# Kernel optimization log

Measured on AMD Instinct MI355X. Metric: run time of the kernel, lower is better.

Reference implementation:

```python
import jax, jax.numpy as jnp
import numpy as np

N = 10000          # nodes
E = 160000         # edges (before self-loops)
F_IN = 256
H, C = 8, 64       # heads, channels per head
NUM_CLASSES = 40
NEG_SLOPE = 0.2    # PyG GATConv default leaky_relu slope


def setup_inputs() -> dict:
    key = jax.random.key(0)
    ks = jax.random.split(key, 16)
    s = 0.1  # keep logits tame
    x = jax.random.normal(ks[0], (N, F_IN), jnp.float32)
    edge_index = jax.random.randint(ks[1], (2, E), 0, N)
    W0 = jax.random.normal(ks[2], (F_IN, H * C), jnp.float32) / np.sqrt(F_IN)
    a_src0 = jax.random.normal(ks[3], (H, C), jnp.float32) * s
    a_dst0 = jax.random.normal(ks[4], (H, C), jnp.float32) * s
    b0 = jnp.zeros((H * C,), jnp.float32)
    W1 = jax.random.normal(ks[5], (H * C, H * C), jnp.float32) / np.sqrt(H * C)
    a_src1 = jax.random.normal(ks[6], (H, C), jnp.float32) * s
    a_dst1 = jax.random.normal(ks[7], (H, C), jnp.float32) * s
    b1 = jnp.zeros((H * C,), jnp.float32)
    W2 = jax.random.normal(ks[8], (H * C, NUM_CLASSES), jnp.float32) / np.sqrt(H * C)
    a_src2 = jax.random.normal(ks[9], (1, NUM_CLASSES), jnp.float32) * s
    a_dst2 = jax.random.normal(ks[10], (1, NUM_CLASSES), jnp.float32) * s
    b2 = jnp.zeros((NUM_CLASSES,), jnp.float32)
    return dict(x=x, edge_index=edge_index, W0=W0, a_src0=a_src0, a_dst0=a_dst0, b0=b0,
                W1=W1, a_src1=a_src1, a_dst1=a_dst1, b1=b1,
                W2=W2, a_src2=a_src2, a_dst2=a_dst2, b2=b2)


def gat_conv(x, src, dst, W, a_src, a_dst, b, concat):
    """PyG GATConv (eval mode: dropout = identity)."""
    n = x.shape[0]
    h, c = a_src.shape
    hx = (x @ W).reshape(n, h, c)                       # [N,H,C]
    al_s = jnp.sum(hx * a_src, axis=-1)                 # [N,H]
    al_d = jnp.sum(hx * a_dst, axis=-1)                 # [N,H]
    e = jax.nn.leaky_relu(al_s[src] + al_d[dst], NEG_SLOPE)  # [E,H]
    # neighbor softmax over incoming edges of each dst node
    m = jax.ops.segment_max(e, dst, num_segments=n)     # [N,H]
    ex = jnp.exp(e - m[dst])
    denom = jax.ops.segment_sum(ex, dst, num_segments=n)
    alpha = ex / (denom[dst] + 1e-16)                   # [E,H]
    msg = hx[src] * alpha[:, :, None]                   # [E,H,C]
    out = jax.ops.segment_sum(msg, dst, num_segments=n) # [N,H,C]
    out = out.reshape(n, h * c) if concat else out.mean(axis=1)
    return out + b


def reference(x, edge_index, W0, a_src0, a_dst0, b0, W1, a_src1, a_dst1, b1,
              W2, a_src2, a_dst2, b2):
    # add self-loops once (PyG GATConv add_self_loops=True)
    loops = jnp.arange(N, dtype=edge_index.dtype)
    src = jnp.concatenate([edge_index[0], loops])
    dst = jnp.concatenate([edge_index[1], loops])
    x = jax.nn.elu(gat_conv(x, src, dst, W0, a_src0, a_dst0, b0, True))
    x = jax.nn.elu(gat_conv(x, src, dst, W1, a_src1, a_dst1, b1, True))
    return gat_conv(x, src, dst, W2, a_src2, a_dst2, b2, False)
```

## Files before the change

### kernel.cpp

```cpp
#include <hip/hip_runtime.h>
#include <math.h>

#define NN 10000
#define EE 160000
#define ET 170000
#define FIN 256
#define HH 8
#define HC 512
#define NCLS 40
#define ELLW 96

typedef _Float16 f16;
using f16x8 = __attribute__((ext_vector_type(8))) _Float16;
using f32x4 = __attribute__((ext_vector_type(4))) float;

#define MFMA16(a, b, c) __builtin_amdgcn_mfma_f32_16x16x32_f16((a), (b), (c), 0, 0, 0)

__device__ __forceinline__ void fmamix2(float& alo, float& ahi, unsigned pk, float w) {
    asm("v_fma_mix_f32 %0, %1, %2, %0 op_sel:[0,0,0] op_sel_hi:[1,0,0]"
        : "+v"(alo) : "v"(pk), "v"(w));
    asm("v_fma_mix_f32 %0, %1, %2, %0 op_sel:[1,0,0] op_sel_hi:[1,0,0]"
        : "+v"(ahi) : "v"(pk), "v"(w));
}

__global__ __launch_bounds__(256) void prep0(const float* __restrict__ W0,
                                             f16* __restrict__ w0T,
                                             int* __restrict__ cnt) {
    int i = blockIdx.x * 256 + threadIdx.x;
    if (i < NN) cnt[i] = 0;
    if (i < HC * FIN) {
        int n = i >> 8, k = i & 255;
        w0T[i] = (f16)W0[(size_t)k * HC + n];
    }
}

__global__ __launch_bounds__(512) void mega0(const float* __restrict__ x,
                                             const f16* __restrict__ w0T,
                                             const float* __restrict__ a_src,
                                             const float* __restrict__ a_dst,
                                             const int* __restrict__ ei,
                                             const float* __restrict__ W1,
                                             const float* __restrict__ W2,
                                             f16* __restrict__ hx2,
                                             float* __restrict__ al_s,
                                             float* __restrict__ al_d,
                                             int* __restrict__ cnt,
                                             int* __restrict__ ell,
                                             f16* __restrict__ w1T,
                                             f16* __restrict__ w2T) {
    __shared__ f16 Bs[64 * FIN];
    int b = blockIdx.x;
    int t = threadIdx.x;
    if (b >= 316) {
        if (b < 649) {
            int e = (b - 316) * 512 + t;
            if (e < ET) {
                int s, d;
                if (e < EE) { s = ei[e]; d = ei[EE + e]; }
                else        { s = e - EE; d = s; }
                int pos = atomicAdd(&cnt[d], 1);
                if (pos < ELLW) ell[(size_t)d * ELLW + pos] = s;
            }
        } else if (b < 1161) {
            int j = (b - 649) * 512 + t;
            int n = j >> 9, k = j & 511;
            w1T[j] = (f16)W1[(size_t)k * HC + n];
        } else {
            int j = (b - 1161) * 512 + t;
            if (j < NCLS * HC) {
                int n = j >> 9, k = j & 511;
                w2T[j] = (f16)W2[(size_t)k * NCLS + n];
            }
        }
        return;
    }
    int hp = b & 3, chunk = b >> 2;
    int lane = t & 63, w = t >> 6;
    int fm = lane & 15, g = lane >> 4;
    int bm = chunk * 128 + w * 16;
    int row = bm + fm;
    bool rok = row < NN;

    f16x8 af[8];
#pragma unroll
    for (int kk = 0; kk < 8; ++kk) {
        float4 lo = make_float4(0.f, 0.f, 0.f, 0.f), hi = lo;
        if (rok) {
            const float* ap = x + (size_t)row * FIN + kk * 32 + g * 8;
            lo = *(const float4*)ap;
            hi = *(const float4*)(ap + 4);
        }
        f16x8 v;
        v[0] = (f16)lo.x; v[1] = (f16)lo.y; v[2] = (f16)lo.z; v[3] = (f16)lo.w;
        v[4] = (f16)hi.x; v[5] = (f16)hi.y; v[6] = (f16)hi.z; v[7] = (f16)hi.w;
        af[kk] = v;
    }

    for (int sl = 0; sl < 2; ++sl) {
        int h = hp * 2 + sl;
        const f16* bsrc = w0T + (size_t)h * 64 * FIN;
        for (int c = t; c < 64 * 32; c += 512) {
            int brow = c >> 5, j = c & 31;
            uint4 v = *(const uint4*)(bsrc + (size_t)brow * FIN + j * 8);
            *(uint4*)&Bs[(size_t)brow * FIN + ((j ^ (brow & 7)) * 8)] = v;
        }
        __syncthreads();

        f32x4 acc[4] = {};
#pragma unroll
        for (int kk = 0; kk < 8; ++kk) {
#pragma unroll
            for (int nt = 0; nt < 4; ++nt) {
                f16x8 bb = *(const f16x8*)
                    &Bs[(nt * 16 + fm) * FIN + (((kk * 4 + g) ^ (fm & 7)) * 8)];
                acc[nt] = MFMA16(af[kk], bb, acc[nt]);
            }
        }

        float asc[4], adc[4];
#pragma unroll
        for (int nt = 0; nt < 4; ++nt) {
            asc[nt] = a_src[h * 64 + nt * 16 + fm];
            adc[nt] = a_dst[h * 64 + nt * 16 + fm];
        }
#pragma unroll
        for (int r = 0; r < 4; ++r) {
            int orow = bm + g * 4 + r;
            float s = acc[0][r] * asc[0] + acc[1][r] * asc[1] +
                      acc[2][r] * asc[2] + acc[3][r] * asc[3];
            float d = acc[0][r] * adc[0] + acc[1][r] * adc[1] +
                      acc[2][r] * adc[2] + acc[3][r] * adc[3];
#pragma unroll
            for (int off = 1; off < 16; off <<= 1) {
                s += __shfl_xor(s, off);
                d += __shfl_xor(d, off);
            }
            if (orow < NN) {
                if (fm == 0) {
                    al_s[orow * 8 + h] = s;
                    al_d[orow * 8 + h] = d;
                }
#pragma unroll
                for (int nt = 0; nt < 4; ++nt)
                    hx2[(size_t)orow * HC + h * 64 + nt * 16 + fm] =
                        (f16)acc[nt][r];
            }
        }
        __syncthreads();
    }
}

template <int K>
__global__ __launch_bounds__(512) void gemm_attn(const f16* __restrict__ A,
                                                 const f16* __restrict__ BT,
                                                 const float* __restrict__ a_src,
                                                 const float* __restrict__ a_dst,
                                                 f16* __restrict__ hx2,
                                                 float* __restrict__ al_s,
                                                 float* __restrict__ al_d) {
    constexpr int KK = K / 32;
    constexpr int CH = K / 8;
    __shared__ f16 Bs[64 * K];
    int t = threadIdx.x;
    int hp = blockIdx.x;
    int lane = t & 63, w = t >> 6;
    int fm = lane & 15, g = lane >> 4;
    int bm = blockIdx.y * 128 + w * 16;
    int row = bm + fm;
    bool rok = row < NN;

    f16x8 af[KK];
#pragma unroll
    for (int kk = 0; kk < KK; ++kk) {
        uint4 r = rok ? *(const uint4*)(A + (size_t)row * K + kk * 32 + g * 8)
                      : make_uint4(0u, 0u, 0u, 0u);
        af[kk] = __builtin_bit_cast(f16x8, r);
    }

    for (int sl = 0; sl < 2; ++sl) {
        int h = hp * 2 + sl;
        const f16* bsrc = BT + (size_t)h * 64 * K;
        for (int c = t; c < 64 * CH; c += 512) {
            int brow = c / CH;
            int j = c - brow * CH;
            uint4 v = *(const uint4*)(bsrc + (size_t)brow * K + j * 8);
            *(uint4*)&Bs[(size_t)brow * K + ((j ^ (brow & 7)) * 8)] = v;
        }
        __syncthreads();

        f32x4 acc[4] = {};
#pragma unroll
        for (int kk = 0; kk < KK; ++kk) {
#pragma unroll
            for (int nt = 0; nt < 4; ++nt) {
                f16x8 b = *(const f16x8*)
                    &Bs[(nt * 16 + fm) * K + (((kk * 4 + g) ^ (fm & 7)) * 8)];
                acc[nt] = MFMA16(af[kk], b, acc[nt]);
            }
        }

        float asc[4], adc[4];
#pragma unroll
        for (int nt = 0; nt < 4; ++nt) {
            asc[nt] = a_src[h * 64 + nt * 16 + fm];
            adc[nt] = a_dst[h * 64 + nt * 16 + fm];
        }
#pragma unroll
        for (int r = 0; r < 4; ++r) {
            int orow = bm + g * 4 + r;
            float s = acc[0][r] * asc[0] + acc[1][r] * asc[1] +
                      acc[2][r] * asc[2] + acc[3][r] * asc[3];
            float d = acc[0][r] * adc[0] + acc[1][r] * adc[1] +
                      acc[2][r] * adc[2] + acc[3][r] * adc[3];
#pragma unroll
            for (int off = 1; off < 16; off <<= 1) {
                s += __shfl_xor(s, off);
                d += __shfl_xor(d, off);
            }
            if (orow < NN) {
                if (fm == 0) {
                    al_s[orow * 8 + h] = s;
                    al_d[orow * 8 + h] = d;
                }
#pragma unroll
                for (int nt = 0; nt < 4; ++nt)
                    hx2[(size_t)orow * HC + h * 64 + nt * 16 + fm] =
                        (f16)acc[nt][r];
            }
        }
        __syncthreads();
    }
}

__global__ __launch_bounds__(256) void gemm2_attn(const f16* __restrict__ A,
                                                  const f16* __restrict__ BT,
                                                  const float* __restrict__ a_src2,
                                                  const float* __restrict__ a_dst2,
                                                  float* __restrict__ hx40,
                                                  float* __restrict__ als2,
                                                  float* __restrict__ ald2) {
    __shared__ f16 Bs[48 * HC];
    int t = threadIdx.x;
    int lane = t & 63, w = t >> 6;
    int fm = lane & 15, g = lane >> 4;
    int bm = blockIdx.x * 64 + w * 16;
    int row = bm + fm;
    bool rok = row < NN;

    for (int c = t; c < 48 * 64; c += 256) {
        int brow = c >> 6, j = c & 63;
        uint4 v = make_uint4(0u, 0u, 0u, 0u);
        if (brow < NCLS) v = *(const uint4*)(BT + (size_t)brow * HC + j * 8);
        *(uint4*)&Bs[brow * HC + ((j ^ (brow & 7)) * 8)] = v;
    }

    f16x8 af[16];
#pragma unroll
    for (int kk = 0; kk < 16; ++kk) {
        uint4 r = rok ? *(const uint4*)(A + (size_t)row * HC + kk * 32 + g * 8)
                      : make_uint4(0u, 0u, 0u, 0u);
        af[kk] = __builtin_bit_cast(f16x8, r);
    }
    __syncthreads();

    f32x4 acc[3] = {};
#pragma unroll
    for (int kk = 0; kk < 16; ++kk) {
#pragma unroll
        for (int nt = 0; nt < 3; ++nt) {
            f16x8 b = *(const f16x8*)
                &Bs[(nt * 16 + fm) * HC + (((kk * 4 + g) ^ (fm & 7)) * 8)];
            acc[nt] = MFMA16(af[kk], b, acc[nt]);
        }
    }

    float a2s[3], a2d[3];
#pragma unroll
    for (int nt = 0; nt < 3; ++nt) {
        int col = nt * 16 + fm;
        a2s[nt] = (col < NCLS) ? a_src2[col] : 0.f;
        a2d[nt] = (col < NCLS) ? a_dst2[col] : 0.f;
    }
#pragma unroll
    for (int r = 0; r < 4; ++r) {
        int orow = bm + g * 4 + r;
        float s = acc[0][r] * a2s[0] + acc[1][r] * a2s[1] + acc[2][r] * a2s[2];
        float d = acc[0][r] * a2d[0] + acc[1][r] * a2d[1] + acc[2][r] * a2d[2];
#pragma unroll
        for (int off = 1; off < 16; off <<= 1) {
            s += __shfl_xor(s, off);
            d += __shfl_xor(d, off);
        }
        if (orow < NN) {
            if (fm == 0) { als2[orow] = s; ald2[orow] = d; }
#pragma unroll
            for (int nt = 0; nt < 3; ++nt) {
                int col = nt * 16 + fm;
                if (col < NCLS) hx40[(size_t)orow * NCLS + col] = acc[nt][r];
            }
        }
    }
}

__global__ __launch_bounds__(256) void agg_ell(const f16* __restrict__ hx2,
                                               const float* __restrict__ al_s,
                                               const float* __restrict__ al_d,
                                               const int* __restrict__ cnt,
                                               const int* __restrict__ ell,
                                               const float* __restrict__ bias,
                                               f16* __restrict__ outF) {
    __shared__ float accbuf[2][64][8];
    __shared__ float denbuf[2][64];
    int t = threadIdx.x;
    int lane = t & 63, w = t >> 6;
    int p = w >> 1, sub = w & 1;
    int n = blockIdx.x * 2 + p;
    bool nok = n < NN;
    int ch = lane * 8;
    int h = lane >> 3;
    float acc[8] = {0.f, 0.f, 0.f, 0.f, 0.f, 0.f, 0.f, 0.f};
    float den = 0.f;
    if (nok) {
        float ald = al_d[n * HH + h];
        int dg = cnt[n]; if (dg > ELLW) dg = ELLW;
        const int* ep = ell + (size_t)n * ELLW;
        int nq = dg >> 2;
        for (int q = sub; q < nq; q += 2) {
            int4 ss = *(const int4*)(ep + (q << 2));
            float e0 = al_s[ss.x * HH + h], e1 = al_s[ss.y * HH + h];
            float e2 = al_s[ss.z * HH + h], e3 = al_s[ss.w * HH + h];
            uint4 v0 = *(const uint4*)(hx2 + (size_t)ss.x * HC + ch);
            uint4 v1 = *(const uint4*)(hx2 + (size_t)ss.y * HC + ch);
            uint4 v2 = *(const uint4*)(hx2 + (size_t)ss.z * HC + ch);
            uint4 v3 = *(const uint4*)(hx2 + (size_t)ss.w * HC + ch);
            e0 += ald; e0 = e0 > 0.f ? e0 : 0.2f * e0;
            e1 += ald; e1 = e1 > 0.f ? e1 : 0.2f * e1;
            e2 += ald; e2 = e2 > 0.f ? e2 : 0.2f * e2;
            e3 += ald; e3 = e3 > 0.f ? e3 : 0.2f * e3;
            float w0 = __expf(e0), w1 = __expf(e1);
            float w2 = __expf(e2), w3 = __expf(e3);
            unsigned q0[4] = {v0.x, v0.y, v0.z, v0.w};
            unsigned q1[4] = {v1.x, v1.y, v1.z, v1.w};
            unsigned q2[4] = {v2.x, v2.y, v2.z, v2.w};
            unsigned q3[4] = {v3.x, v3.y, v3.z, v3.w};
#pragma unroll
            for (int j = 0; j < 4; ++j) {
                fmamix2(acc[2 * j], acc[2 * j + 1], q0[j], w0);
                fmamix2(acc[2 * j], acc[2 * j + 1], q1[j], w1);
                fmamix2(acc[2 * j], acc[2 * j + 1], q2[j], w2);
                fmamix2(acc[2 * j], acc[2 * j + 1], q3[j], w3);
            }
            den += w0 + w1 + w2 + w3;
        }
        if (sub == (nq & 1)) {
            for (int i2 = nq << 2; i2 < dg; ++i2) {
                int s = ep[i2];
                float e = al_s[s * HH + h] + ald;
                e = e > 0.f ? e : 0.2f * e;
                float wgt = __expf(e);
                uint4 v = *(const uint4*)(hx2 + (size_t)s * HC + ch);
                unsigned qq[4] = {v.x, v.y, v.z, v.w};
#pragma unroll
                for (int j = 0; j < 4; ++j)
                    fmamix2(acc[2 * j], acc[2 * j + 1], qq[j], wgt);
                den += wgt;
            }
        }
    }
    if (sub == 1) {
#pragma unroll
        for (int j = 0; j < 8; ++j) accbuf[p][lane][j] = acc[j];
        denbuf[p][lane] = den;
    }
    __syncthreads();
    if (sub == 0 && nok) {
#pragma unroll
        for (int j = 0; j < 8; ++j) acc[j] += accbuf[p][lane][j];
        den += denbuf[p][lane];
        float inv = 1.f / (den + 1e-16f);
        float4 b0v = *(const float4*)(bias + ch);
        float4 b1v = *(const float4*)(bias + ch + 4);
        float bb[8] = {b0v.x, b0v.y, b0v.z, b0v.w, b1v.x, b1v.y, b1v.z, b1v.w};
        f16x8 o;
#pragma unroll
        for (int j = 0; j < 8; ++j) {
            float v = acc[j] * inv + bb[j];
            v = v > 0.f ? v : expm1f(v);
            o[j] = (f16)v;
        }
        *(uint4*)(outF + (size_t)n * HC + ch) = __builtin_bit_cast(uint4, o);
    }
}

__global__ __launch_bounds__(256) void agg2_final(const float* __restrict__ hx40,
                                                  const float* __restrict__ als,
                                                  const float* __restrict__ aldp,
                                                  const int* __restrict__ cnt,
                                                  const int* __restrict__ ell,
                                                  const float* __restrict__ b2,
                                                  float* __restrict__ out) {
    int t = threadIdx.x;
    int n = blockIdx.x * 4 + (t >> 6);
    int c = t & 63;
    if (n >= NN) return;
    float ald = aldp[n];
    int dg = cnt[n]; if (dg > ELLW) dg = ELLW;
    const int* ep = ell + (size_t)n * ELLW;
    float acc = 0.f, den = 0.f;
    int i = 0;
    for (; i + 4 <= dg; i += 4) {
        int4 ss = *(const int4*)(ep + i);
        float e0 = als[ss.x], e1 = als[ss.y], e2 = als[ss.z], e3 = als[ss.w];
        float v0 = 0.f, v1 = 0.f, v2 = 0.f, v3 = 0.f;
        if (c < NCLS) {
            v0 = hx40[(size_t)ss.x * NCLS + c];
            v1 = hx40[(size_t)ss.y * NCLS + c];
            v2 = hx40[(size_t)ss.z * NCLS + c];
            v3 = hx40[(size_t)ss.w * NCLS + c];
        }
        e0 += ald; e0 = e0 > 0.f ? e0 : 0.2f * e0;
        e1 += ald; e1 = e1 > 0.f ? e1 : 0.2f * e1;
        e2 += ald; e2 = e2 > 0.f ? e2 : 0.2f * e2;
        e3 += ald; e3 = e3 > 0.f ? e3 : 0.2f * e3;
        float w0 = __expf(e0), w1 = __expf(e1), w2 = __expf(e2), w3 = __expf(e3);
        acc += w0 * v0 + w1 * v1 + w2 * v2 + w3 * v3;
        den += w0 + w1 + w2 + w3;
    }
    for (; i < dg; ++i) {
        int s = ep[i];
        float e = als[s] + ald;
        e = e > 0.f ? e : 0.2f * e;
        float wgt = __expf(e);
        if (c < NCLS) acc += wgt * hx40[(size_t)s * NCLS + c];
        den += wgt;
    }
    if (c < NCLS) out[(size_t)n * NCLS + c] = acc / (den + 1e-16f) + b2[c];
}

extern "C" void kernel_launch(void* const* d_in, const int* in_sizes, int n_in,
                              void* d_out, int out_size, void* d_ws, size_t ws_size,
                              hipStream_t stream) {
    const float* x   = (const float*)d_in[0];
    const int*   ei  = (const int*)  d_in[1];
    const float* W0  = (const float*)d_in[2];
    const float* as0 = (const float*)d_in[3];
    const float* ad0 = (const float*)d_in[4];
    const float* b0  = (const float*)d_in[5];
    const float* W1  = (const float*)d_in[6];
    const float* as1 = (const float*)d_in[7];
    const float* ad1 = (const float*)d_in[8];
    const float* b1  = (const float*)d_in[9];
    const float* W2  = (const float*)d_in[10];
    const float* as2 = (const float*)d_in[11];
    const float* ad2 = (const float*)d_in[12];
    const float* b2  = (const float*)d_in[13];
    float* out = (float*)d_out;

    char* p = (char*)d_ws;
    int* cnt  = (int*)p; p += 40064;
    int* ell  = (int*)p; p += (size_t)NN * ELLW * 4;
    f16* w0T  = (f16*)p; p += HC * FIN * 2;
    f16* w1T  = (f16*)p; p += HC * HC * 2;
    f16* w2T  = (f16*)p; p += NCLS * HC * 2;
    f16* hxA  = (f16*)p; p += (size_t)NN * HC * 2;
    f16* hxB  = (f16*)p; p += (size_t)NN * HC * 2;
    f16* fA   = (f16*)p; p += (size_t)NN * HC * 2;
    f16* fB   = (f16*)p; p += (size_t)NN * HC * 2;
    float* hx40 = (float*)p; p += (size_t)NN * NCLS * 4;
    float* als0 = (float*)p; p += NN * HH * 4;
    float* ald0 = (float*)p; p += NN * HH * 4;
    float* als1 = (float*)p; p += NN * HH * 4;
    float* ald1 = (float*)p; p += NN * HH * 4;
    float* als2 = (float*)p; p += NN * 4;
    float* ald2 = (float*)p; p += NN * 4;

    const int NBR = (NN + 127) / 128;
    const int NAG = (NN + 1) / 2;
    const int NB2 = (NN + 63) / 64;

    prep0<<<(HC * FIN + 255) / 256, 256, 0, stream>>>(W0, w0T, cnt);
    mega0<<<1201, 512, 0, stream>>>(x, w0T, as0, ad0, ei, W1, W2,
                                    hxA, als0, ald0, cnt, ell, w1T, w2T);
    agg_ell<<<NAG, 256, 0, stream>>>(hxA, als0, ald0, cnt, ell, b0, fA);
    dim3 gA(4, NBR);
    gemm_attn<HC><<<gA, 512, 0, stream>>>(fA, w1T, as1, ad1, hxB, als1, ald1);
    agg_ell<<<NAG, 256, 0, stream>>>(hxB, als1, ald1, cnt, ell, b1, fB);
    gemm2_attn<<<NB2, 256, 0, stream>>>(fB, w2T, as2, ad2, hx40, als2, ald2);
    agg2_final<<<(NN + 3) / 4, 256, 0, stream>>>(hx40, als2, ald2, cnt, ell, b2, out);
}
```

Baseline: 199.3 us.

## Fuse aggregation with following GEMM via per-chunk completion counters

Merges each ELL aggregation kernel with the following dense GEMM+attention kernel into one launch. Aggregation blocks (4 nodes each, 512 threads) bump a per-128-row chunk counter, and GEMM blocks spin on that counter before consuming the rows, so the GEMM can start on finished chunks while aggregation continues. This removes two kernel launches and the drain gaps between them. The cost is spin-wait polling, a reliance on aggregation blocks being scheduled before the waiting GEMM blocks, and the GEMM staging its weights in two K-halves to fit the shared-memory union.

After: 465.4 us. +133.5%, slower.

```diff
diff --git a/kernel.cpp b/kernel.cpp
--- a/kernel.cpp
+++ b/kernel.cpp
@@ -9,6 +9,8 @@
 #define HC 512
 #define NCLS 40
 #define ELLW 96
+#define NAGB 2500
+#define NCH 79
 
 typedef _Float16 f16;
 using f16x8 = __attribute__((ext_vector_type(8))) _Float16;
@@ -25,9 +27,12 @@
 
 __global__ __launch_bounds__(256) void prep0(const float* __restrict__ W0,
                                              f16* __restrict__ w0T,
-                                             int* __restrict__ cnt) {
+                                             int* __restrict__ cnt,
+                                             int* __restrict__ cd1,
+                                             int* __restrict__ cd2) {
     int i = blockIdx.x * 256 + threadIdx.x;
     if (i < NN) cnt[i] = 0;
+    if (i < NCH) { cd1[i] = 0; cd2[i] = 0; }
     if (i < HC * FIN) {
         int n = i >> 8, k = i & 255;
         w0T[i] = (f16)W0[(size_t)k * HC + n];
@@ -150,233 +155,84 @@
     }
 }
 
-template <int K>
-__global__ __launch_bounds__(512) void gemm_attn(const f16* __restrict__ A,
-                                                 const f16* __restrict__ BT,
-                                                 const float* __restrict__ a_src,
-                                                 const float* __restrict__ a_dst,
-                                                 f16* __restrict__ hx2,
-                                                 float* __restrict__ al_s,
-                                                 float* __restrict__ al_d) {
-    constexpr int KK = K / 32;
-    constexpr int CH = K / 8;
-    __shared__ f16 Bs[64 * K];
-    int t = threadIdx.x;
-    int hp = blockIdx.x;
-    int lane = t & 63, w = t >> 6;
-    int fm = lane & 15, g = lane >> 4;
-    int bm = blockIdx.y * 128 + w * 16;
-    int row = bm + fm;
-    bool rok = row < NN;
-
-    f16x8 af[KK];
-#pragma unroll
-    for (int kk = 0; kk < KK; ++kk) {
-        uint4 r = rok ? *(const uint4*)(A + (size_t)row * K + kk * 32 + g * 8)
-                      : make_uint4(0u, 0u, 0u, 0u);
-        af[kk] = __builtin_bit_cast(f16x8, r);
-    }
-
-    for (int sl = 0; sl < 2; ++sl) {
-        int h = hp * 2 + sl;
-        const f16* bsrc = BT + (size_t)h * 64 * K;
-        for (int c = t; c < 64 * CH; c += 512) {
-            int brow = c / CH;
-            int j = c - brow * CH;
-            uint4 v = *(const uint4*)(bsrc + (size_t)brow * K + j * 8);
-            *(uint4*)&Bs[(size_t)brow * K + ((j ^ (brow & 7)) * 8)] = v;
-        }
-        __syncthreads();
-
-        f32x4 acc[4] = {};
-#pragma unroll
-        for (int kk = 0; kk < KK; ++kk) {
-#pragma unroll
-            for (int nt = 0; nt < 4; ++nt) {
-                f16x8 b = *(const f16x8*)
-                    &Bs[(nt * 16 + fm) * K + (((kk * 4 + g) ^ (fm & 7)) * 8)];
-                acc[nt] = MFMA16(af[kk], b, acc[nt]);
-            }
-        }
-
-        float asc[4], adc[4];
-#pragma unroll
-        for (int nt = 0; nt < 4; ++nt) {
-            asc[nt] = a_src[h * 64 + nt * 16 + fm];
-            adc[nt] = a_dst[h * 64 + nt * 16 + fm];
-        }
-#pragma unroll
-        for (int r = 0; r < 4; ++r) {
-            int orow = bm + g * 4 + r;
-            float s = acc[0][r] * asc[0] + acc[1][r] * asc[1] +
-                      acc[2][r] * asc[2] + acc[3][r] * asc[3];
-            float d = acc[0][r] * adc[0] + acc[1][r] * adc[1] +
-                      acc[2][r] * adc[2] + acc[3][r] * adc[3];
-#pragma unroll
-            for (int off = 1; off < 16; off <<= 1) {
-                s += __shfl_xor(s, off);
-                d += __shfl_xor(d, off);
-            }
-            if (orow < NN) {
-                if (fm == 0) {
-                    al_s[orow * 8 + h] = s;
-                    al_d[orow * 8 + h] = d;
-                }
-#pragma unroll
-                for (int nt = 0; nt < 4; ++nt)
-                    hx2[(size_t)orow * HC + h * 64 + nt * 16 + fm] =
-                        (f16)acc[nt][r];
-            }
-        }
-        __syncthreads();
-    }
-}
-
-__global__ __launch_bounds__(256) void gemm2_attn(const f16* __restrict__ A,
-                                                  const f16* __restrict__ BT,
-                                                  const float* __restrict__ a_src2,
-                                                  const float* __restrict__ a_dst2,
-                                                  float* __restrict__ hx40,
-                                                  float* __restrict__ als2,
-                                                  float* __restrict__ ald2) {
-    __shared__ f16 Bs[48 * HC];
-    int t = threadIdx.x;
-    int lane = t & 63, w = t >> 6;
-    int fm = lane & 15, g = lane >> 4;
-    int bm = blockIdx.x * 64 + w * 16;
-    int row = bm + fm;
-    bool rok = row < NN;
-
-    for (int c = t; c < 48 * 64; c += 256) {
-        int brow = c >> 6, j = c & 63;
-        uint4 v = make_uint4(0u, 0u, 0u, 0u);
-        if (brow < NCLS) v = *(const uint4*)(BT + (size_t)brow * HC + j * 8);
-        *(uint4*)&Bs[brow * HC + ((j ^ (brow & 7)) * 8)] = v;
-    }
-
-    f16x8 af[16];
-#pragma unroll
-    for (int kk = 0; kk < 16; ++kk) {
-        uint4 r = rok ? *(const uint4*)(A + (size_t)row * HC + kk * 32 + g * 8)
-                      : make_uint4(0u, 0u, 0u, 0u);
-        af[kk] = __builtin_bit_cast(f16x8, r);
-    }
-    __syncthreads();
-
-    f32x4 acc[3] = {};
-#pragma unroll
-    for (int kk = 0; kk < 16; ++kk) {
-#pragma unroll
-        for (int nt = 0; nt < 3; ++nt) {
-            f16x8 b = *(const f16x8*)
-                &Bs[(nt * 16 + fm) * HC + (((kk * 4 + g) ^ (fm & 7)) * 8)];
-            acc[nt] = MFMA16(af[kk], b, acc[nt]);
-        }
-    }
-
-    float a2s[3], a2d[3];
-#pragma unroll
-    for (int nt = 0; nt < 3; ++nt) {
-        int col = nt * 16 + fm;
-        a2s[nt] = (col < NCLS) ? a_src2[col] : 0.f;
-        a2d[nt] = (col < NCLS) ? a_dst2[col] : 0.f;
-    }
-#pragma unroll
-    for (int r = 0; r < 4; ++r) {
-        int orow = bm + g * 4 + r;
-        float s = acc[0][r] * a2s[0] + acc[1][r] * a2s[1] + acc[2][r] * a2s[2];
-        float d = acc[0][r] * a2d[0] + acc[1][r] * a2d[1] + acc[2][r] * a2d[2];
-#pragma unroll
-        for (int off = 1; off < 16; off <<= 1) {
-            s += __shfl_xor(s, off);
-            d += __shfl_xor(d, off);
-        }
-        if (orow < NN) {
-            if (fm == 0) { als2[orow] = s; ald2[orow] = d; }
-#pragma unroll
-            for (int nt = 0; nt < 3; ++nt) {
-                int col = nt * 16 + fm;
-                if (col < NCLS) hx40[(size_t)orow * NCLS + col] = acc[nt][r];
-            }
-        }
-    }
-}
-
-__global__ __launch_bounds__(256) void agg_ell(const f16* __restrict__ hx2,
-                                               const float* __restrict__ al_s,
-                                               const float* __restrict__ al_d,
-                                               const int* __restrict__ cnt,
-                                               const int* __restrict__ ell,
-                                               const float* __restrict__ bias,
-                                               f16* __restrict__ outF) {
-    __shared__ float accbuf[2][64][8];
-    __shared__ float denbuf[2][64];
+struct SM {
+    union {
+        f16 Bs[64 * 256];
+        struct { float ab[4][64][8]; float db[4][64]; } a;
+    } u;
+};
+
+__device__ __forceinline__ void agg_body(SM& sm,
+                                         const f16* __restrict__ hx2,
+                                         const float* __restrict__ al_s,
+                                         const float* __restrict__ al_d,
+                                         const int* __restrict__ cnt,
+                                         const int* __restrict__ ell,
+                                         const float* __restrict__ bias,
+                                         f16* __restrict__ outF, int b) {
     int t = threadIdx.x;
     int lane = t & 63, w = t >> 6;
     int p = w >> 1, sub = w & 1;
-    int n = blockIdx.x * 2 + p;
-    bool nok = n < NN;
+    int n = b * 4 + p;
     int ch = lane * 8;
     int h = lane >> 3;
     float acc[8] = {0.f, 0.f, 0.f, 0.f, 0.f, 0.f, 0.f, 0.f};
     float den = 0.f;
-    if (nok) {
-        float ald = al_d[n * HH + h];
-        int dg = cnt[n]; if (dg > ELLW) dg = ELLW;
-        const int* ep = ell + (size_t)n * ELLW;
-        int nq = dg >> 2;
-        for (int q = sub; q < nq; q += 2) {
-            int4 ss = *(const int4*)(ep + (q << 2));
-            float e0 = al_s[ss.x * HH + h], e1 = al_s[ss.y * HH + h];
-            float e2 = al_s[ss.z * HH + h], e3 = al_s[ss.w * HH + h];
-            uint4 v0 = *(const uint4*)(hx2 + (size_t)ss.x * HC + ch);
-            uint4 v1 = *(const uint4*)(hx2 + (size_t)ss.y * HC + ch);
-            uint4 v2 = *(const uint4*)(hx2 + (size_t)ss.z * HC + ch);
-            uint4 v3 = *(const uint4*)(hx2 + (size_t)ss.w * HC + ch);
-            e0 += ald; e0 = e0 > 0.f ? e0 : 0.2f * e0;
-            e1 += ald; e1 = e1 > 0.f ? e1 : 0.2f * e1;
-            e2 += ald; e2 = e2 > 0.f ? e2 : 0.2f * e2;
-            e3 += ald; e3 = e3 > 0.f ? e3 : 0.2f * e3;
-            float w0 = __expf(e0), w1 = __expf(e1);
-            float w2 = __expf(e2), w3 = __expf(e3);
-            unsigned q0[4] = {v0.x, v0.y, v0.z, v0.w};
-            unsigned q1[4] = {v1.x, v1.y, v1.z, v1.w};
-            unsigned q2[4] = {v2.x, v2.y, v2.z, v2.w};
-            unsigned q3[4] = {v3.x, v3.y, v3.z, v3.w};
-#pragma unroll
-            for (int j = 0; j < 4; ++j) {
-                fmamix2(acc[2 * j], acc[2 * j + 1], q0[j], w0);
-                fmamix2(acc[2 * j], acc[2 * j + 1], q1[j], w1);
-                fmamix2(acc[2 * j], acc[2 * j + 1], q2[j], w2);
-                fmamix2(acc[2 * j], acc[2 * j + 1], q3[j], w3);
-            }
-            den += w0 + w1 + w2 + w3;
-        }
-        if (sub == (nq & 1)) {
-            for (int i2 = nq << 2; i2 < dg; ++i2) {
-                int s = ep[i2];
-                float e = al_s[s * HH + h] + ald;
-                e = e > 0.f ? e : 0.2f * e;
-                float wgt = __expf(e);
-                uint4 v = *(const uint4*)(hx2 + (size_t)s * HC + ch);
-                unsigned qq[4] = {v.x, v.y, v.z, v.w};
-#pragma unroll
-                for (int j = 0; j < 4; ++j)
-                    fmamix2(acc[2 * j], acc[2 * j + 1], qq[j], wgt);
-                den += wgt;
-            }
+    float ald = al_d[n * HH + h];
+    int dg = cnt[n]; if (dg > ELLW) dg = ELLW;
+    const int* ep = ell + (size_t)n * ELLW;
+    int nq = dg >> 2;
+    for (int q = sub; q < nq; q += 2) {
+        int4 ss = *(const int4*)(ep + (q << 2));
+        float e0 = al_s[ss.x * HH + h], e1 = al_s[ss.y * HH + h];
+        float e2 = al_s[ss.z * HH + h], e3 = al_s[ss.w * HH + h];
+        uint4 v0 = *(const uint4*)(hx2 + (size_t)ss.x * HC + ch);
+        uint4 v1 = *(const uint4*)(hx2 + (size_t)ss.y * HC + ch);
+        uint4 v2 = *(const uint4*)(hx2 + (size_t)ss.z * HC + ch);
+        uint4 v3 = *(const uint4*)(hx2 + (size_t)ss.w * HC + ch);
+        e0 += ald; e0 = e0 > 0.f ? e0 : 0.2f * e0;
+        e1 += ald; e1 = e1 > 0.f ? e1 : 0.2f * e1;
+        e2 += ald; e2 = e2 > 0.f ? e2 : 0.2f * e2;
+        e3 += ald; e3 = e3 > 0.f ? e3 : 0.2f * e3;
+        float w0 = __expf(e0), w1 = __expf(e1);
+        float w2 = __expf(e2), w3 = __expf(e3);
+        unsigned q0[4] = {v0.x, v0.y, v0.z, v0.w};
+        unsigned q1[4] = {v1.x, v1.y, v1.z, v1.w};
+        unsigned q2[4] = {v2.x, v2.y, v2.z, v2.w};
+        unsigned q3[4] = {v3.x, v3.y, v3.z, v3.w};
+#pragma unroll
+        for (int j = 0; j < 4; ++j) {
+            fmamix2(acc[2 * j], acc[2 * j + 1], q0[j], w0);
+            fmamix2(acc[2 * j], acc[2 * j + 1], q1[j], w1);
+            fmamix2(acc[2 * j], acc[2 * j + 1], q2[j], w2);
+            fmamix2(acc[2 * j], acc[2 * j + 1], q3[j], w3);
+        }
+        den += w0 + w1 + w2 + w3;
+    }
+    if (sub == (nq & 1)) {
+        for (int i2 = nq << 2; i2 < dg; ++i2) {
+            int s = ep[i2];
+            float e = al_s[s * HH + h] + ald;
+            e = e > 0.f ? e : 0.2f * e;
+            float wgt = __expf(e);
+            uint4 v = *(const uint4*)(hx2 + (size_t)s * HC + ch);
+            unsigned qq[4] = {v.x, v.y, v.z, v.w};
+#pragma unroll
+            for (int j = 0; j < 4; ++j)
+                fmamix2(acc[2 * j], acc[2 * j + 1], qq[j], wgt);
+            den += wgt;
         }
     }
     if (sub == 1) {
 #pragma unroll
-        for (int j = 0; j < 8; ++j) accbuf[p][lane][j] = acc[j];
-        denbuf[p][lane] = den;
+        for (int j = 0; j < 8; ++j) sm.u.a.ab[p][lane][j] = acc[j];
+        sm.u.a.db[p][lane] = den;
     }
     __syncthreads();
-    if (sub == 0 && nok) {
-#pragma unroll
-        for (int j = 0; j < 8; ++j) acc[j] += accbuf[p][lane][j];
-        den += denbuf[p][lane];
+    if (sub == 0) {
+#pragma unroll
+        for (int j = 0; j < 8; ++j) acc[j] += sm.u.a.ab[p][lane][j];
+        den += sm.u.a.db[p][lane];
         float inv = 1.f / (den + 1e-16f);
         float4 b0v = *(const float4*)(bias + ch);
         float4 b1v = *(const float4*)(bias + ch + 4);
@@ -389,6 +245,211 @@
             o[j] = (f16)v;
         }
         *(uint4*)(outF + (size_t)n * HC + ch) = __builtin_bit_cast(uint4, o);
+    }
+    __syncthreads();
+}
+
+__global__ __launch_bounds__(512, 4) void fused1(const f16* __restrict__ hxA,
+                                                 const float* __restrict__ als0,
+                                                 const float* __restrict__ ald0,
+                                                 const int* __restrict__ cnt,
+                                                 const int* __restrict__ ell,
+                                                 const float* __restrict__ b0,
+                                                 f16* __restrict__ fA,
+                                                 const f16* __restrict__ w1T,
+                                                 const float* __restrict__ as1,
+                                                 const float* __restrict__ ad1,
+                                                 f16* __restrict__ hxB,
+                                                 float* __restrict__ als1,
+                                                 float* __restrict__ ald1,
+                                                 int* __restrict__ cd) {
+    __shared__ SM sm;
+    int b = blockIdx.x;
+    int t = threadIdx.x;
+    if (b < NAGB) {
+        agg_body(sm, hxA, als0, ald0, cnt, ell, b0, fA, b);
+        if (t == 0) {
+            __threadfence();
+            atomicAdd(&cd[b >> 5], 1);
+        }
+        return;
+    }
+    int c = b - NAGB;
+    int hp = c & 3, chunk = c >> 2;
+    int target = NAGB - 32 * chunk; if (target > 32) target = 32;
+    if (t == 0) {
+        while (__hip_atomic_load(&cd[chunk], __ATOMIC_RELAXED,
+                                 __HIP_MEMORY_SCOPE_AGENT) < target)
+            __builtin_amdgcn_s_sleep(8);
+    }
+    __syncthreads();
+    __threadfence();
+    int lane = t & 63, w = t >> 6;
+    int fm = lane & 15, g = lane >> 4;
+    int bm = chunk * 128 + w * 16;
+    int row = bm + fm;
+    bool rok = row < NN;
+
+    f32x4 acc[2][4] = {};
+    for (int kh = 0; kh < 2; ++kh) {
+        f16x8 af[8];
+#pragma unroll
+        for (int kk = 0; kk < 8; ++kk) {
+            uint4 r = rok ? *(const uint4*)(fA + (size_t)row * HC + kh * 256 +
+                                            kk * 32 + g * 8)
+                          : make_uint4(0u, 0u, 0u, 0u);
+            af[kk] = __builtin_bit_cast(f16x8, r);
+        }
+        for (int sl = 0; sl < 2; ++sl) {
+            int h2 = hp * 2 + sl;
+            const f16* bsrc = w1T + (size_t)h2 * 64 * HC + kh * 256;
+            __syncthreads();
+            for (int cc = t; cc < 64 * 32; cc += 512) {
+                int brow = cc >> 5, j = cc & 31;
+                uint4 v = *(const uint4*)(bsrc + (size_t)brow * HC + j * 8);
+                *(uint4*)&sm.u.Bs[brow * 256 + ((j ^ (brow & 7)) * 8)] = v;
+            }
+            __syncthreads();
+#pragma unroll
+            for (int kk = 0; kk < 8; ++kk) {
+#pragma unroll
+                for (int nt = 0; nt < 4; ++nt) {
+                    f16x8 bb = *(const f16x8*)
+                        &sm.u.Bs[(nt * 16 + fm) * 256 + (((kk * 4 + g) ^ (fm & 7)) * 8)];
+                    acc[sl][nt] = MFMA16(af[kk], bb, acc[sl][nt]);
+                }
+            }
+        }
+    }
+#pragma unroll
+    for (int sl = 0; sl < 2; ++sl) {
+        int h2 = hp * 2 + sl;
+        float asc[4], adc[4];
+#pragma unroll
+        for (int nt = 0; nt < 4; ++nt) {
+            asc[nt] = as1[h2 * 64 + nt * 16 + fm];
+            adc[nt] = ad1[h2 * 64 + nt * 16 + fm];
+        }
+#pragma unroll
+        for (int r = 0; r < 4; ++r) {
+            int orow = bm + g * 4 + r;
+            float s = acc[sl][0][r] * asc[0] + acc[sl][1][r] * asc[1] +
+                      acc[sl][2][r] * asc[2] + acc[sl][3][r] * asc[3];
+            float d = acc[sl][0][r] * adc[0] + acc[sl][1][r] * adc[1] +
+                      acc[sl][2][r] * adc[2] + acc[sl][3][r] * adc[3];
+#pragma unroll
+            for (int off = 1; off < 16; off <<= 1) {
+                s += __shfl_xor(s, off);
+                d += __shfl_xor(d, off);
+            }
+            if (orow < NN) {
+                if (fm == 0) {
+                    als1[orow * 8 + h2] = s;
+                    ald1[orow * 8 + h2] = d;
+                }
+#pragma unroll
+                for (int nt = 0; nt < 4; ++nt)
+                    hxB[(size_t)orow * HC + h2 * 64 + nt * 16 + fm] =
+                        (f16)acc[sl][nt][r];
+            }
+        }
+    }
+}
+
+__global__ __launch_bounds__(512, 4) void fused2(const f16* __restrict__ hxB,
+                                                 const float* __restrict__ als1,
+                                                 const float* __restrict__ ald1,
+                                                 const int* __restrict__ cnt,
+                                                 const int* __restrict__ ell,
+                                                 const float* __restrict__ b1,
+                                                 f16* __restrict__ fB,
+                                                 const f16* __restrict__ w2T,
+                                                 const float* __restrict__ as2,
+                                                 const float* __restrict__ ad2,
+                                                 float* __restrict__ hx40,
+                                                 float* __restrict__ als2,
+                                                 float* __restrict__ ald2,
+                                                 int* __restrict__ cd) {
+    __shared__ SM sm;
+    int b = blockIdx.x;
+    int t = threadIdx.x;
+    if (b < NAGB) {
+        agg_body(sm, hxB, als1, ald1, cnt, ell, b1, fB, b);
+        if (t == 0) {
+            __threadfence();
+            atomicAdd(&cd[b >> 5], 1);
+        }
+        return;
+    }
+    int chunk = b - NAGB;
+    int target = NAGB - 32 * chunk; if (target > 32) target = 32;
+    if (t == 0) {
+        while (__hip_atomic_load(&cd[chunk], __ATOMIC_RELAXED,
+                                 __HIP_MEMORY_SCOPE_AGENT) < target)
+            __builtin_amdgcn_s_sleep(8);
+    }
+    __syncthreads();
+    __threadfence();
+    int lane = t & 63, w = t >> 6;
+    int fm = lane & 15, g = lane >> 4;
+    int bm = chunk * 128 + w * 16;
+    int row = bm + fm;
+    bool rok = row < NN;
+
+    f32x4 acc[3] = {};
+    for (int kh = 0; kh < 2; ++kh) {
+        f16x8 af[8];
+#pragma unroll
+        for (int kk = 0; kk < 8; ++kk) {
+            uint4 r = rok ? *(const uint4*)(fB + (size_t)row * HC + kh * 256 +
+                                            kk * 32 + g * 8)
+                          : make_uint4(0u, 0u, 0u, 0u);
+            af[kk] = __builtin_bit_cast(f16x8, r);
+        }
+        __syncthreads();
+        for (int cc = t; cc < 48 * 32; cc += 512) {
+            int brow = cc >> 5, j = cc & 31;
+            uint4 v = make_uint4(0u, 0u, 0u, 0u);
+            if (brow < NCLS)
+                v = *(const uint4*)(w2T + (size_t)brow * HC + kh * 256 + j * 8);
+            *(uint4*)&sm.u.Bs[brow * 256 + ((j ^ (brow & 7)) * 8)] = v;
+        }
+        __syncthreads();
+#pragma unroll
+        for (int kk = 0; kk < 8; ++kk) {
+#pragma unroll
+            for (int nt = 0; nt < 3; ++nt) {
+                f16x8 bb = *(const f16x8*)
+                    &sm.u.Bs[(nt * 16 + fm) * 256 + (((kk * 4 + g) ^ (fm & 7)) * 8)];
+                acc[nt] = MFMA16(af[kk], bb, acc[nt]);
+            }
+        }
+    }
+    float a2s[3], a2d[3];
+#pragma unroll
+    for (int nt = 0; nt < 3; ++nt) {
+        int col = nt * 16 + fm;
+        a2s[nt] = (col < NCLS) ? as2[col] : 0.f;
+        a2d[nt] = (col < NCLS) ? ad2[col] : 0.f;
+    }
+#pragma unroll
+    for (int r = 0; r < 4; ++r) {
+        int orow = bm + g * 4 + r;
+        float s = acc[0][r] * a2s[0] + acc[1][r] * a2s[1] + acc[2][r] * a2s[2];
+        float d = acc[0][r] * a2d[0] + acc[1][r] * a2d[1] + acc[2][r] * a2d[2];
+#pragma unroll
+        for (int off = 1; off < 16; off <<= 1) {
+            s += __shfl_xor(s, off);
+            d += __shfl_xor(d, off);
+        }
+        if (orow < NN) {
+            if (fm == 0) { als2[orow] = s; ald2[orow] = d; }
+#pragma unroll
+            for (int nt = 0; nt < 3; ++nt) {
+                int col = nt * 16 + fm;
+                if (col < NCLS) hx40[(size_t)orow * NCLS + col] = acc[nt][r];
+            }
+        }
     }
 }
 
@@ -458,6 +519,8 @@
 
     char* p = (char*)d_ws;
     int* cnt  = (int*)p; p += 40064;
+    int* cd1  = (int*)p; p += 512;
+    int* cd2  = (int*)p; p += 512;
     int* ell  = (int*)p; p += (size_t)NN * ELLW * 4;
     f16* w0T  = (f16*)p; p += HC * FIN * 2;
     f16* w1T  = (f16*)p; p += HC * HC * 2;
@@ -474,17 +537,12 @@
     float* als2 = (float*)p; p += NN * 4;
     float* ald2 = (float*)p; p += NN * 4;
 
-    const int NBR = (NN + 127) / 128;
-    const int NAG = (NN + 1) / 2;
-    const int NB2 = (NN + 63) / 64;
-
-    prep0<<<(HC * FIN + 255) / 256, 256, 0, stream>>>(W0, w0T, cnt);
+    prep0<<<(HC * FIN + 255) / 256, 256, 0, stream>>>(W0, w0T, cnt, cd1, cd2);
     mega0<<<1201, 512, 0, stream>>>(x, w0T, as0, ad0, ei, W1, W2,
                                     hxA, als0, ald0, cnt, ell, w1T, w2T);
-    agg_ell<<<NAG, 256, 0, stream>>>(hxA, als0, ald0, cnt, ell, b0, fA);
-    dim3 gA(4, NBR);
-    gemm_attn<HC><<<gA, 512, 0, stream>>>(fA, w1T, as1, ad1, hxB, als1, ald1);
-    agg_ell<<<NAG, 256, 0, stream>>>(hxB, als1, ald1, cnt, ell, b1, fB);
-    gemm2_attn<<<NB2, 256, 0, stream>>>(fB, w2T, as2, ad2, hx40, als2, ald2);
+    fused1<<<NAGB + 316, 512, 0, stream>>>(hxA, als0, ald0, cnt, ell, b0, fA,
+                                           w1T, as1, ad1, hxB, als1, ald1, cd1);
+    fused2<<<NAGB + NCH, 512, 0, stream>>>(hxB, als1, ald1, cnt, ell, b1, fB,
+                                           w2T, as2, ad2, hx40, als2, ald2, cd2);
     agg2_final<<<(NN + 3) / 4, 256, 0, stream>>>(hx40, als2, ald2, cnt, ell, b2, out);
 }
```
